# Performance work log

Measured on AMD Instinct MI355X. Metric: run time of the kernel, lower is better.

The kernel has to match this reference:

```python
import jax, jax.numpy as jnp
import numpy as np

ALPHA = 0.2  # LeakyReLU negative slope (init arg `alpha`)
N, F_IN, F_OUT = 8192, 512, 256


def setup_inputs() -> dict:
    key = jax.random.key(0)
    k1, k2, k3, k4 = jax.random.split(key, 4)
    x = jax.random.normal(k1, (N, F_IN), dtype=jnp.float32)
    adj = jax.random.randint(k2, (N, N), 0, 2, dtype=jnp.int32)
    W = jax.random.normal(k3, (F_IN, F_OUT), dtype=jnp.float32) * (1.0 / np.sqrt(F_IN))
    a = jax.random.normal(k4, (2 * F_OUT, 1), dtype=jnp.float32) * (1.0 / np.sqrt(F_IN))
    return {"x": x, "adj": adj, "W": W, "a": a}


def reference(x, adj, W, a):
    h = x @ W  # [N, F_OUT]
    f_out = W.shape[1]
    # e[i,j] = LeakyReLU(a1 . h_i + a2 . h_j); computed without the O(N^2*2F) concat
    f1 = h @ a[:f_out, 0]   # [N]
    f2 = h @ a[f_out:, 0]   # [N]
    s = f1[:, None] + f2[None, :]  # [N, N]
    e = jnp.where(s >= 0, s, ALPHA * s)
    # Faithful to the source bug: -9e15 * zeros_like == zeros, so masked entries are 0.0
    att = jnp.where(adj > 0, e, jnp.zeros((), dtype=e.dtype))
    att = jax.nn.softmax(att, axis=1)
    # dropout is identity in eval mode
    h_prime = att @ h  # [N, F_OUT]
    return jax.nn.elu(h_prime)  # concat=True branch
```

## Files before the change

kernel.cpp:

```cpp
#include <hip/hip_runtime.h>
#include <stdint.h>

#define NN 8192
#define FIN 512
#define FOUT 256
#define ALPHA 0.2f
#define KSPLIT 4

typedef float f32x4 __attribute__((ext_vector_type(4)));
typedef short s16x8 __attribute__((ext_vector_type(8)));

__device__ __forceinline__ uint16_t f2bf(float f) {
  union { float f; uint32_t u; } v; v.f = f;
  uint32_t u = v.u + 0x7fffu + ((v.u >> 16) & 1u);
  return (uint16_t)(u >> 16);
}

__global__ __launch_bounds__(256) void k_wa_prep(const float* __restrict__ W,
                                                 const float* __restrict__ a,
                                                 uint16_t* __restrict__ wt,
                                                 float* __restrict__ wa1, float* __restrict__ wa2) {
  int bx = blockIdx.x;
  int tid = threadIdx.x;
  if (bx < 128) {
    int idx = bx * 256 + tid;
    int f  = idx >> 7;
    int k4 = (idx & 127) * 4;
    ushort4 o;
    o.x = f2bf(W[(size_t)(k4 + 0) * FOUT + f]);
    o.y = f2bf(W[(size_t)(k4 + 1) * FOUT + f]);
    o.z = f2bf(W[(size_t)(k4 + 2) * FOUT + f]);
    o.w = f2bf(W[(size_t)(k4 + 3) * FOUT + f]);
    *(ushort4*)(wt + (size_t)f * FIN + k4) = o;
  } else {
    __shared__ float a1[256], a2[256];
    a1[tid] = a[tid];
    a2[tid] = a[tid + 256];
    __syncthreads();
    int m = (bx - 128) * 256 + tid;
    const float* wrow = W + (size_t)m * FOUT;
    float s1 = 0.f, s2 = 0.f;
    for (int k = 0; k < FOUT; k += 4) {
      f32x4 v = *(const f32x4*)(wrow + k);
#pragma unroll
      for (int i = 0; i < 4; i++) {
        s1 += v[i] * a1[k + i];
        s2 += v[i] * a2[k + i];
      }
    }
    wa1[m] = s1; wa2[m] = s2;
  }
}

__global__ __launch_bounds__(256) void k_f1f2(const float* __restrict__ x,
                                              const float* __restrict__ wa1,
                                              const float* __restrict__ wa2,
                                              float* __restrict__ f1, float* __restrict__ f2,
                                              uint16_t* __restrict__ xb,
                                              float* __restrict__ l_arr) {
  __shared__ float s1[512], s2[512];
  int tid = threadIdx.x;
  if (tid < 4) l_arr[blockIdx.x * 4 + tid] = 0.f;
  s1[tid] = wa1[tid]; s1[tid + 256] = wa1[tid + 256];
  s2[tid] = wa2[tid]; s2[tid + 256] = wa2[tid + 256];
  __syncthreads();
  int w = tid >> 6, l = tid & 63;
  int row = blockIdx.x * 4 + w;
  const float* xr = x + (size_t)row * FIN + l * 8;
  f32x4 v0 = *(const f32x4*)xr;
  f32x4 v1 = *(const f32x4*)(xr + 4);
  uint4 pk;
  pk.x = (uint32_t)f2bf(v0[0]) | ((uint32_t)f2bf(v0[1]) << 16);
  pk.y = (uint32_t)f2bf(v0[2]) | ((uint32_t)f2bf(v0[3]) << 16);
  pk.z = (uint32_t)f2bf(v1[0]) | ((uint32_t)f2bf(v1[1]) << 16);
  pk.w = (uint32_t)f2bf(v1[2]) | ((uint32_t)f2bf(v1[3]) << 16);
  *(uint4*)(xb + (size_t)row * FIN + l * 8) = pk;
  int kb = l * 8;
  float d1 = 0.f, d2 = 0.f;
#pragma unroll
  for (int i = 0; i < 4; i++) {
    d1 += v0[i] * s1[kb + i] + v1[i] * s1[kb + 4 + i];
    d2 += v0[i] * s2[kb + i] + v1[i] * s2[kb + 4 + i];
  }
#pragma unroll
  for (int off = 32; off; off >>= 1) {
    d1 += __shfl_down(d1, off);
    d2 += __shfl_down(d2, off);
  }
  if (l == 0) { f1[row] = d1; f2[row] = d2; }
}

__global__ __launch_bounds__(256, 2) void k_gemm_ht(const uint16_t* __restrict__ xb,
                                                    const uint16_t* __restrict__ wt,
                                                    uint16_t* __restrict__ ht) {
  __shared__ uint16_t Xs[64][72];
  __shared__ uint16_t Ws[64][72];
  __shared__ uint16_t T[64][72];
  int i0 = blockIdx.x * 64;
  int f0 = blockIdx.y * 64;
  int tid = threadIdx.x;
  int w = tid >> 6, l = tid & 63;
  int q = l >> 4, r16 = l & 15;
  f32x4 acc[4];
#pragma unroll
  for (int b = 0; b < 4; b++) acc[b] = (f32x4)0.f;

  int srow = tid >> 2, sch = tid & 3;
  for (int k0 = 0; k0 < FIN; k0 += 64) {
    const uint16_t* xp = xb + (size_t)(i0 + srow) * FIN + k0;
    const uint16_t* wp = wt + (size_t)(f0 + srow) * FIN + k0;
    uint4 xv0 = *(const uint4*)(xp + sch * 8);
    uint4 xv1 = *(const uint4*)(xp + 32 + sch * 8);
    uint4 wv0 = *(const uint4*)(wp + sch * 8);
    uint4 wv1 = *(const uint4*)(wp + 32 + sch * 8);
    *(uint4*)(&Xs[srow][sch * 8]) = xv0;
    *(uint4*)(&Xs[srow][32 + sch * 8]) = xv1;
    *(uint4*)(&Ws[srow][sch * 8]) = wv0;
    *(uint4*)(&Ws[srow][32 + sch * 8]) = wv1;
    __syncthreads();
#pragma unroll
    for (int c = 0; c < 2; c++) {
      s16x8 A = *(const s16x8*)(&Xs[w * 16 + r16][c * 32 + q * 8]);
      s16x8 B[4];
#pragma unroll
      for (int b = 0; b < 4; b++) B[b] = *(const s16x8*)(&Ws[b * 16 + r16][c * 32 + q * 8]);
#pragma unroll
      for (int b = 0; b < 4; b++)
        acc[b] = __builtin_amdgcn_mfma_f32_16x16x32_bf16(A, B[b], acc[b], 0, 0, 0);
    }
    __syncthreads();
  }
#pragma unroll
  for (int b = 0; b < 4; b++)
#pragma unroll
    for (int reg = 0; reg < 4; reg++)
      T[w * 16 + q * 4 + reg][b * 16 + r16] = f2bf(acc[b][reg]);
  __syncthreads();
#pragma unroll
  for (int p = 0; p < 2; p++) {
    int idx = tid + p * 256;
    int fr = idx >> 3, ic8 = idx & 7;
    s16x8 v;
#pragma unroll
    for (int j = 0; j < 8; j++) v[j] = (short)T[ic8 * 8 + j][fr];
    *(s16x8*)(ht + (size_t)(f0 + fr) * NN + i0 + ic8 * 8) = v;
  }
}

__global__ __launch_bounds__(256, 2) void k_att(const int* __restrict__ adj,
                                                const uint16_t* __restrict__ ht,
                                                const float* __restrict__ f1,
                                                const float* __restrict__ f2,
                                                float* __restrict__ l_arr,
                                                float* __restrict__ part) {
  __shared__ uint16_t Ps[64][72];
  __shared__ uint16_t Hs[256][72];
  int i0 = blockIdx.x * 64;
  int jbase = blockIdx.y * (NN / KSPLIT);
  int tid = threadIdx.x;
  int w = tid >> 6, l = tid & 63;
  int q = l >> 4, r16 = l & 15;
  int prow = tid >> 2, pch = tid & 3;
  int srow = tid >> 3, sch = tid & 7;
  float f1i = f1[i0 + prow];
  float lsum = 0.f;
  f32x4 acc[4][4];
#pragma unroll
  for (int a = 0; a < 4; a++)
#pragma unroll
    for (int b = 0; b < 4; b++) acc[a][b] = (f32x4)0.f;

  for (int s = 0; s < NN / KSPLIT; s += 64) {
    int j0 = jbase + s;
    uint4 hv[8];
#pragma unroll
    for (int p = 0; p < 8; p++)
      hv[p] = *(const uint4*)(ht + (size_t)(p * 32 + srow) * NN + j0 + sch * 8);
    const int* ap = adj + (size_t)(i0 + prow) * NN + j0 + pch * 16;
    int4 A0 = *(const int4*)ap;
    int4 A1 = *(const int4*)(ap + 4);
    int4 A2 = *(const int4*)(ap + 8);
    int4 A3 = *(const int4*)(ap + 12);
    f32x4 F0 = *(const f32x4*)(f2 + j0 + pch * 16);
    f32x4 F1 = *(const f32x4*)(f2 + j0 + pch * 16 + 4);
    f32x4 F2 = *(const f32x4*)(f2 + j0 + pch * 16 + 8);
    f32x4 F3 = *(const f32x4*)(f2 + j0 + pch * 16 + 12);
    s16x8 pv0, pv1;
#define PCOMP(dst, Ac, Fc, kk) { float s_ = f1i + (Fc); float e_ = s_ > 0.f ? s_ : ALPHA * s_; \
                                 float p_ = ((Ac) != 0) ? __expf(e_) : 1.0f; lsum += p_; \
                                 dst[kk] = (short)f2bf(p_); }
    PCOMP(pv0, A0.x, F0[0], 0); PCOMP(pv0, A0.y, F0[1], 1);
    PCOMP(pv0, A0.z, F0[2], 2); PCOMP(pv0, A0.w, F0[3], 3);
    PCOMP(pv0, A1.x, F1[0], 4); PCOMP(pv0, A1.y, F1[1], 5);
    PCOMP(pv0, A1.z, F1[2], 6); PCOMP(pv0, A1.w, F1[3], 7);
    PCOMP(pv1, A2.x, F2[0], 0); PCOMP(pv1, A2.y, F2[1], 1);
    PCOMP(pv1, A2.z, F2[2], 2); PCOMP(pv1, A2.w, F2[3], 3);
    PCOMP(pv1, A3.x, F3[0], 4); PCOMP(pv1, A3.y, F3[1], 5);
    PCOMP(pv1, A3.z, F3[2], 6); PCOMP(pv1, A3.w, F3[3], 7);
#undef PCOMP
    *(s16x8*)(&Ps[prow][pch * 16]) = pv0;
    *(s16x8*)(&Ps[prow][pch * 16 + 8]) = pv1;
#pragma unroll
    for (int p = 0; p < 8; p++)
      *(uint4*)(&Hs[p * 32 + srow][sch * 8]) = hv[p];
    __syncthreads();
#pragma unroll
    for (int c = 0; c < 2; c++) {
      s16x8 Af[4], Bf[4];
#pragma unroll
      for (int a = 0; a < 4; a++) Af[a] = *(const s16x8*)(&Ps[a * 16 + r16][c * 32 + q * 8]);
#pragma unroll
      for (int b = 0; b < 4; b++) Bf[b] = *(const s16x8*)(&Hs[w * 64 + b * 16 + r16][c * 32 + q * 8]);
#pragma unroll
      for (int a = 0; a < 4; a++)
#pragma unroll
        for (int b = 0; b < 4; b++)
          acc[a][b] = __builtin_amdgcn_mfma_f32_16x16x32_bf16(Af[a], Bf[b], acc[a][b], 0, 0, 0);
    }
    __syncthreads();
  }

  lsum += __shfl_down(lsum, 2);
  lsum += __shfl_down(lsum, 1);
  if (pch == 0) atomicAdd(&l_arr[i0 + prow], lsum);

  float* pb = part + (size_t)blockIdx.y * ((size_t)NN * FOUT);
#pragma unroll
  for (int a = 0; a < 4; a++)
#pragma unroll
    for (int b = 0; b < 4; b++)
#pragma unroll
      for (int reg = 0; reg < 4; reg++) {
        int row = i0 + a * 16 + q * 4 + reg;
        int col = w * 64 + b * 16 + r16;
        pb[(size_t)row * FOUT + col] = acc[a][b][reg];
      }
}

__global__ __launch_bounds__(256) void k_combine(const float* __restrict__ part,
                                                 const float* __restrict__ l_arr,
                                                 float* __restrict__ out) {
  int idx = (blockIdx.x * 256 + threadIdx.x) * 4;
  float r = 1.0f / l_arr[idx >> 8];
  f32x4 v0 = __builtin_nontemporal_load((const f32x4*)(part + 0 * (size_t)(NN * FOUT) + idx));
  f32x4 v1 = __builtin_nontemporal_load((const f32x4*)(part + 1 * (size_t)(NN * FOUT) + idx));
  f32x4 v2 = __builtin_nontemporal_load((const f32x4*)(part + 2 * (size_t)(NN * FOUT) + idx));
  f32x4 v3 = __builtin_nontemporal_load((const f32x4*)(part + 3 * (size_t)(NN * FOUT) + idx));
  f32x4 o;
#pragma unroll
  for (int i = 0; i < 4; i++) {
    float v = (v0[i] + v1[i] + v2[i] + v3[i]) * r;
    o[i] = v > 0.f ? v : (__expf(v) - 1.f);
  }
  __builtin_nontemporal_store(o, (f32x4*)(out + idx));
}

extern "C" void kernel_launch(void* const* d_in, const int* in_sizes, int n_in,
                              void* d_out, int out_size, void* d_ws, size_t ws_size,
                              hipStream_t stream) {
  const float* x   = (const float*)d_in[0];
  const int*   adj = (const int*)d_in[1];
  const float* W   = (const float*)d_in[2];
  const float* a   = (const float*)d_in[3];
  float* out = (float*)d_out;

  char* ws = (char*)d_ws;
  float*    wa1   = (float*)ws;
  float*    wa2   = wa1 + 512;
  float*    f1    = wa2 + 512;
  float*    f2    = f1 + NN;
  float*    l_arr = f2 + NN;
  uint16_t* wt    = (uint16_t*)(l_arr + NN);
  uint16_t* xb    = wt + (size_t)FOUT * FIN;
  uint16_t* ht    = xb + (size_t)NN * FIN;
  float*    part  = (float*)(ht + (size_t)NN * FOUT);

  k_wa_prep<<<130, 256, 0, stream>>>(W, a, wt, wa1, wa2);
  k_f1f2<<<NN / 4, 256, 0, stream>>>(x, wa1, wa2, f1, f2, xb, l_arr);
  k_gemm_ht<<<dim3(NN / 64, FOUT / 64), 256, 0, stream>>>(xb, wt, ht);
  k_att<<<dim3(NN / 64, KSPLIT), 256, 0, stream>>>(adj, ht, f1, f2, l_arr, part);
  k_combine<<<NN * FOUT / 1024, 256, 0, stream>>>(part, l_arr, out);
}
```

Before: 437.1 us.

## Double attention row tile to 128 and raise K-split to 8

The attention kernel now processes 128 rows per block instead of 64, with each thread computing 32 attention probabilities, so every staged tile of the transposed h is reused across twice as many rows. This halves the repeated h traffic from L2/HBM per unit of work. The split over the neighbour dimension grows from 4 to 8 to keep the grid size the same, so the combine kernel reads eight partial buffers. That means the partial outputs take twice the memory and bandwidth, and the larger accumulator array (32 MFMA tiles per thread) raises register pressure under the two-blocks-per-CU launch bound.

```diff
diff --git a/kernel.cpp b/kernel.cpp
--- a/kernel.cpp
+++ b/kernel.cpp
@@ -5,7 +5,8 @@
 #define FIN 512
 #define FOUT 256
 #define ALPHA 0.2f
-#define KSPLIT 4
+#define KSPLIT 8
+#define ITILE 128
 
 typedef float f32x4 __attribute__((ext_vector_type(4)));
 typedef short s16x8 __attribute__((ext_vector_type(8)));
@@ -153,20 +154,20 @@
                                                 const float* __restrict__ f2,
                                                 float* __restrict__ l_arr,
                                                 float* __restrict__ part) {
-  __shared__ uint16_t Ps[64][72];
+  __shared__ uint16_t Ps[128][72];
   __shared__ uint16_t Hs[256][72];
-  int i0 = blockIdx.x * 64;
+  int i0 = blockIdx.x * ITILE;
   int jbase = blockIdx.y * (NN / KSPLIT);
   int tid = threadIdx.x;
   int w = tid >> 6, l = tid & 63;
   int q = l >> 4, r16 = l & 15;
-  int prow = tid >> 2, pch = tid & 3;
+  int prow = tid >> 1, pch = tid & 1;
   int srow = tid >> 3, sch = tid & 7;
   float f1i = f1[i0 + prow];
   float lsum = 0.f;
-  f32x4 acc[4][4];
-#pragma unroll
-  for (int a = 0; a < 4; a++)
+  f32x4 acc[8][4];
+#pragma unroll
+  for (int a = 0; a < 8; a++)
 #pragma unroll
     for (int b = 0; b < 4; b++) acc[a][b] = (f32x4)0.f;
 
@@ -176,57 +177,51 @@
 #pragma unroll
     for (int p = 0; p < 8; p++)
       hv[p] = *(const uint4*)(ht + (size_t)(p * 32 + srow) * NN + j0 + sch * 8);
-    const int* ap = adj + (size_t)(i0 + prow) * NN + j0 + pch * 16;
-    int4 A0 = *(const int4*)ap;
-    int4 A1 = *(const int4*)(ap + 4);
-    int4 A2 = *(const int4*)(ap + 8);
-    int4 A3 = *(const int4*)(ap + 12);
-    f32x4 F0 = *(const f32x4*)(f2 + j0 + pch * 16);
-    f32x4 F1 = *(const f32x4*)(f2 + j0 + pch * 16 + 4);
-    f32x4 F2 = *(const f32x4*)(f2 + j0 + pch * 16 + 8);
-    f32x4 F3 = *(const f32x4*)(f2 + j0 + pch * 16 + 12);
-    s16x8 pv0, pv1;
-#define PCOMP(dst, Ac, Fc, kk) { float s_ = f1i + (Fc); float e_ = s_ > 0.f ? s_ : ALPHA * s_; \
-                                 float p_ = ((Ac) != 0) ? __expf(e_) : 1.0f; lsum += p_; \
-                                 dst[kk] = (short)f2bf(p_); }
-    PCOMP(pv0, A0.x, F0[0], 0); PCOMP(pv0, A0.y, F0[1], 1);
-    PCOMP(pv0, A0.z, F0[2], 2); PCOMP(pv0, A0.w, F0[3], 3);
-    PCOMP(pv0, A1.x, F1[0], 4); PCOMP(pv0, A1.y, F1[1], 5);
-    PCOMP(pv0, A1.z, F1[2], 6); PCOMP(pv0, A1.w, F1[3], 7);
-    PCOMP(pv1, A2.x, F2[0], 0); PCOMP(pv1, A2.y, F2[1], 1);
-    PCOMP(pv1, A2.z, F2[2], 2); PCOMP(pv1, A2.w, F2[3], 3);
-    PCOMP(pv1, A3.x, F3[0], 4); PCOMP(pv1, A3.y, F3[1], 5);
-    PCOMP(pv1, A3.z, F3[2], 6); PCOMP(pv1, A3.w, F3[3], 7);
+    const int* ap = adj + (size_t)(i0 + prow) * NN + j0 + pch * 32;
+    const float* fp = f2 + j0 + pch * 32;
+    s16x8 pv[4];
+#pragma unroll
+    for (int g = 0; g < 4; ++g) {
+      int4 Aa = *(const int4*)(ap + g * 8);
+      int4 Ab = *(const int4*)(ap + g * 8 + 4);
+      f32x4 Fa = *(const f32x4*)(fp + g * 8);
+      f32x4 Fb = *(const f32x4*)(fp + g * 8 + 4);
+#define PCOMP(Ac, Fc, kk) { float s_ = f1i + (Fc); float e_ = s_ > 0.f ? s_ : ALPHA * s_; \
+                            float p_ = ((Ac) != 0) ? __expf(e_) : 1.0f; lsum += p_; \
+                            pv[g][kk] = (short)f2bf(p_); }
+      PCOMP(Aa.x, Fa[0], 0) PCOMP(Aa.y, Fa[1], 1) PCOMP(Aa.z, Fa[2], 2) PCOMP(Aa.w, Fa[3], 3)
+      PCOMP(Ab.x, Fb[0], 4) PCOMP(Ab.y, Fb[1], 5) PCOMP(Ab.z, Fb[2], 6) PCOMP(Ab.w, Fb[3], 7)
 #undef PCOMP
-    *(s16x8*)(&Ps[prow][pch * 16]) = pv0;
-    *(s16x8*)(&Ps[prow][pch * 16 + 8]) = pv1;
+    }
+#pragma unroll
+    for (int g = 0; g < 4; ++g)
+      *(s16x8*)(&Ps[prow][pch * 32 + g * 8]) = pv[g];
 #pragma unroll
     for (int p = 0; p < 8; p++)
       *(uint4*)(&Hs[p * 32 + srow][sch * 8]) = hv[p];
     __syncthreads();
 #pragma unroll
     for (int c = 0; c < 2; c++) {
-      s16x8 Af[4], Bf[4];
-#pragma unroll
-      for (int a = 0; a < 4; a++) Af[a] = *(const s16x8*)(&Ps[a * 16 + r16][c * 32 + q * 8]);
+      s16x8 Bf[4];
 #pragma unroll
       for (int b = 0; b < 4; b++) Bf[b] = *(const s16x8*)(&Hs[w * 64 + b * 16 + r16][c * 32 + q * 8]);
 #pragma unroll
-      for (int a = 0; a < 4; a++)
+      for (int a = 0; a < 8; a++) {
+        s16x8 Af = *(const s16x8*)(&Ps[a * 16 + r16][c * 32 + q * 8]);
 #pragma unroll
         for (int b = 0; b < 4; b++)
-          acc[a][b] = __builtin_amdgcn_mfma_f32_16x16x32_bf16(Af[a], Bf[b], acc[a][b], 0, 0, 0);
-    }
-    __syncthreads();
-  }
-
-  lsum += __shfl_down(lsum, 2);
+          acc[a][b] = __builtin_amdgcn_mfma_f32_16x16x32_bf16(Af, Bf[b], acc[a][b], 0, 0, 0);
+      }
+    }
+    __syncthreads();
+  }
+
   lsum += __shfl_down(lsum, 1);
   if (pch == 0) atomicAdd(&l_arr[i0 + prow], lsum);
 
   float* pb = part + (size_t)blockIdx.y * ((size_t)NN * FOUT);
 #pragma unroll
-  for (int a = 0; a < 4; a++)
+  for (int a = 0; a < 8; a++)
 #pragma unroll
     for (int b = 0; b < 4; b++)
 #pragma unroll
@@ -242,14 +237,14 @@
                                                  float* __restrict__ out) {
   int idx = (blockIdx.x * 256 + threadIdx.x) * 4;
   float r = 1.0f / l_arr[idx >> 8];
-  f32x4 v0 = __builtin_nontemporal_load((const f32x4*)(part + 0 * (size_t)(NN * FOUT) + idx));
-  f32x4 v1 = __builtin_nontemporal_load((const f32x4*)(part + 1 * (size_t)(NN * FOUT) + idx));
-  f32x4 v2 = __builtin_nontemporal_load((const f32x4*)(part + 2 * (size_t)(NN * FOUT) + idx));
-  f32x4 v3 = __builtin_nontemporal_load((const f32x4*)(part + 3 * (size_t)(NN * FOUT) + idx));
+  f32x4 sum = (f32x4)0.f;
+#pragma unroll
+  for (int p = 0; p < KSPLIT; p++)
+    sum += __builtin_nontemporal_load((const f32x4*)(part + (size_t)p * (NN * FOUT) + idx));
   f32x4 o;
 #pragma unroll
   for (int i = 0; i < 4; i++) {
-    float v = (v0[i] + v1[i] + v2[i] + v3[i]) * r;
+    float v = sum[i] * r;
     o[i] = v > 0.f ? v : (__expf(v) - 1.f);
   }
   __builtin_nontemporal_store(o, (f32x4*)(out + idx));
@@ -278,6 +273,6 @@
   k_wa_prep<<<130, 256, 0, stream>>>(W, a, wt, wa1, wa2);
   k_f1f2<<<NN / 4, 256, 0, stream>>>(x, wa1, wa2, f1, f2, xb, l_arr);
   k_gemm_ht<<<dim3(NN / 64, FOUT / 64), 256, 0, stream>>>(xb, wt, ht);
-  k_att<<<dim3(NN / 64, KSPLIT), 256, 0, stream>>>(adj, ht, f1, f2, l_arr, part);
+  k_att<<<dim3(NN / ITILE, KSPLIT), 256, 0, stream>>>(adj, ht, f1, f2, l_arr, part);
   k_combine<<<NN * FOUT / 1024, 256, 0, stream>>>(part, l_arr, out);
 }
```

After: 472.1 us. 8.0% more time.
